# Kernel optimization log

Measured on AMD Instinct MI355X. Metric: run time of the kernel, lower is better.

Reference implementation:

```python
import jax, jax.numpy as jnp
import numpy as np

MX, SX = 0.0, 1.0  # msx
MY, SY = 0.0, 1.0  # msy


def _mode_linear(inp, phase, w, b):
    # Equivalent to: w_p = einsum('ji,imk->jmk', phase, w); out = squeeze(inp[:,None,:] @ w_p) + phase @ b
    # Fused blended form avoids the (batch, in, out) per-sample weight intermediate.
    out = jnp.einsum('bd,idh,bi->bh', inp, w, phase)
    return out + phase @ b


def setup_inputs() -> dict:
    key = jax.random.key(0)
    ks = jax.random.split(key, 4)
    B, D_IN, H, D_OUT = 32768, 256, 1024, 64
    x = jax.random.normal(ks[0], (B, D_IN + 2), dtype=jnp.float32)
    w1 = jax.random.normal(ks[1], (2, D_IN, H), dtype=jnp.float32) * 0.05
    b1 = jnp.zeros((2, H), dtype=jnp.float32)
    w2 = jax.random.normal(ks[2], (2, H, H), dtype=jnp.float32) * 0.05
    b2 = jnp.zeros((2, H), dtype=jnp.float32)
    w3 = jax.random.normal(ks[3], (2, H, D_OUT), dtype=jnp.float32) * 0.05
    b3 = jnp.zeros((2, D_OUT), dtype=jnp.float32)
    return {"x": x, "w1": w1, "b1": b1, "w2": w2, "b2": b2, "w3": w3, "b3": b3}


def reference(x, w1, b1, w2, b2, w3, b3):
    phase = x[:, -2:]                 # unscaled phase weights, per original code
    xs = (x - MX) / SX
    h = xs[:, :-2]                    # [B, D_IN]
    out = jax.nn.elu(_mode_linear(h, phase, w1, b1))
    out = jax.nn.elu(_mode_linear(out, phase, w2, b2))
    out = _mode_linear(out, phase, w3, b3)
    return out * SY + MY
```

## Files before the change

kernel.cpp:

```cpp
#include <hip/hip_runtime.h>

typedef unsigned short u16;
typedef __bf16 bf16x8 __attribute__((ext_vector_type(8)));
typedef float f32x4 __attribute__((ext_vector_type(4)));

static __device__ __forceinline__ u16 f2bf(float f) {
  union { float f; unsigned u; } v; v.f = f;
  unsigned r = (v.u + 0x7fff + ((v.u >> 16) & 1)) >> 16;
  return (u16)r;
}

__global__ void prep_x_kernel(const float* __restrict__ x, u16* __restrict__ hx,
                              float2* __restrict__ phase, int B) {
  int i = blockIdx.x * blockDim.x + threadIdx.x;
  int total = B * 128;
  if (i < total) {
    int row = i >> 7, k2 = (i & 127);
    const float2 v = *reinterpret_cast<const float2*>(x + (size_t)row * 258 + k2 * 2);
    u16 a = f2bf(v.x), b = f2bf(v.y);
    *reinterpret_cast<unsigned*>(hx + (size_t)row * 256 + k2 * 2) =
        (unsigned)a | ((unsigned)b << 16);
  }
  if (i < B) {
    phase[i] = *reinterpret_cast<const float2*>(x + (size_t)i * 258 + 256);
  }
}

__global__ void prep_w_kernel(const float* __restrict__ w, u16* __restrict__ wt,
                              int K, int N) {
  __shared__ u16 tile[64][65];
  int k0 = blockIdx.x * 64, n0 = blockIdx.y * 64, mode = blockIdx.z;
  const float* src = w + (size_t)mode * K * N;
  u16* dst = wt + (size_t)mode * N * K;
  int c = threadIdx.x & 63;
  int r4 = threadIdx.x >> 6;
#pragma unroll
  for (int i = 0; i < 16; ++i) {
    int r = r4 + i * 4;
    tile[r][c] = f2bf(src[(size_t)(k0 + r) * N + n0 + c]);
  }
  __syncthreads();
#pragma unroll
  for (int i = 0; i < 16; ++i) {
    int r = r4 + i * 4;
    dst[(size_t)(n0 + r) * K + k0 + c] = tile[c][r];
  }
}

template <int BM, int BN, int WM, int WN, bool ELU_BF16>
__launch_bounds__(256, 2) __global__
void gemm_dualmode(const u16* __restrict__ A, const u16* __restrict__ WT,
                   const float* __restrict__ bias, const float2* __restrict__ phase,
                   void* __restrict__ out, int K, int N) {
  constexpr int MF = WM / 16, NF = WN / 16;
  __shared__ u16 ldsA[BM * 32];
  __shared__ u16 ldsB[2][BN * 32];
  const int m0 = blockIdx.x * BM;
  const int n0 = blockIdx.y * BN;
  const int t = threadIdx.x;
  const int wave = t >> 6, lane = t & 63;
  constexpr int NWC = BN / WN;
  const int wr = wave / NWC, wc = wave % NWC;
  const int lr = lane & 15, ks = lane >> 4;

  f32x4 acc[2][MF][NF] = {};

  for (int kt = 0; kt < K; kt += 32) {
#pragma unroll
    for (int i = 0; i < BM / 64; ++i) {
      int tt = t + i * 256;
      int r = tt >> 2, c8 = (tt & 3) * 8;
      __builtin_amdgcn_global_load_lds(
          (const __attribute__((address_space(1))) void*)(A + (size_t)(m0 + r) * K + kt + c8),
          (__attribute__((address_space(3))) void*)(ldsA + (size_t)tt * 8), 16, 0, 0);
    }
#pragma unroll
    for (int md = 0; md < 2; ++md) {
#pragma unroll
      for (int i = 0; i < BN / 64; ++i) {
        int tt = t + i * 256;
        int r = tt >> 2, c8 = (tt & 3) * 8;
        __builtin_amdgcn_global_load_lds(
            (const __attribute__((address_space(1))) void*)(WT + (size_t)md * N * K +
                                                            (size_t)(n0 + r) * K + kt + c8),
            (__attribute__((address_space(3))) void*)(ldsB[md] + (size_t)tt * 8), 16, 0, 0);
      }
    }
    __syncthreads();

    bf16x8 af[MF], b0f[NF], b1f[NF];
#pragma unroll
    for (int m = 0; m < MF; ++m)
      af[m] = *reinterpret_cast<const bf16x8*>(&ldsA[(wr * WM + m * 16 + lr) * 32 + ks * 8]);
#pragma unroll
    for (int n = 0; n < NF; ++n) {
      b0f[n] = *reinterpret_cast<const bf16x8*>(&ldsB[0][(wc * WN + n * 16 + lr) * 32 + ks * 8]);
      b1f[n] = *reinterpret_cast<const bf16x8*>(&ldsB[1][(wc * WN + n * 16 + lr) * 32 + ks * 8]);
    }
#pragma unroll
    for (int m = 0; m < MF; ++m) {
#pragma unroll
      for (int n = 0; n < NF; ++n) {
        acc[0][m][n] = __builtin_amdgcn_mfma_f32_16x16x32_bf16(af[m], b0f[n], acc[0][m][n], 0, 0, 0);
        acc[1][m][n] = __builtin_amdgcn_mfma_f32_16x16x32_bf16(af[m], b1f[n], acc[1][m][n], 0, 0, 0);
      }
    }
    __syncthreads();
  }

#pragma unroll
  for (int m = 0; m < MF; ++m) {
#pragma unroll
    for (int j = 0; j < 4; ++j) {
      int grow = m0 + wr * WM + m * 16 + ks * 4 + j;
      float2 ph = phase[grow];
#pragma unroll
      for (int n = 0; n < NF; ++n) {
        int gcol = n0 + wc * WN + n * 16 + lr;
        float v = ph.x * (acc[0][m][n][j] + bias[gcol]) +
                  ph.y * (acc[1][m][n][j] + bias[N + gcol]);
        if (ELU_BF16) {
          v = v > 0.f ? v : (__expf(v) - 1.f);
          ((u16*)out)[(size_t)grow * N + gcol] = f2bf(v);
        } else {
          ((float*)out)[(size_t)grow * N + gcol] = v;
        }
      }
    }
  }
}

extern "C" void kernel_launch(void* const* d_in, const int* in_sizes, int n_in,
                              void* d_out, int out_size, void* d_ws, size_t ws_size,
                              hipStream_t stream) {
  const float* x  = (const float*)d_in[0];
  const float* w1 = (const float*)d_in[1];
  const float* b1 = (const float*)d_in[2];
  const float* w2 = (const float*)d_in[3];
  const float* b2 = (const float*)d_in[4];
  const float* w3 = (const float*)d_in[5];
  const float* b3 = (const float*)d_in[6];
  float* out = (float*)d_out;
  const int B = 32768, DIN = 256, H = 1024, DOUT = 64;

  char* ws = (char*)d_ws;
  u16* W1T = (u16*)ws;     ws += (size_t)2 * H * DIN * 2;
  u16* W2T = (u16*)ws;     ws += (size_t)2 * H * H * 2;
  u16* W3T = (u16*)ws;     ws += (size_t)2 * DOUT * H * 2;
  float2* phase = (float2*)ws; ws += (size_t)B * 8;
  u16* hx = (u16*)ws;      ws += (size_t)B * DIN * 2;
  u16* h1 = (u16*)ws;      ws += (size_t)B * H * 2;
  u16* h2 = (u16*)ws;      ws += (size_t)B * H * 2;

  prep_x_kernel<<<(B * 128 + 255) / 256, 256, 0, stream>>>(x, hx, phase, B);
  prep_w_kernel<<<dim3(DIN / 64, H / 64, 2), 256, 0, stream>>>(w1, W1T, DIN, H);
  prep_w_kernel<<<dim3(H / 64, H / 64, 2), 256, 0, stream>>>(w2, W2T, H, H);
  prep_w_kernel<<<dim3(H / 64, DOUT / 64, 2), 256, 0, stream>>>(w3, W3T, H, DOUT);

  gemm_dualmode<128, 128, 64, 64, true>
      <<<dim3(B / 128, H / 128), 256, 0, stream>>>(hx, W1T, b1, phase, h1, DIN, H);
  gemm_dualmode<128, 128, 64, 64, true>
      <<<dim3(B / 128, H / 128), 256, 0, stream>>>(h1, W2T, b2, phase, h2, H, H);
  gemm_dualmode<128, 64, 64, 32, false>
      <<<dim3(B / 128, DOUT / 64), 256, 0, stream>>>(h2, W3T, b3, phase, out, H, DOUT);
}
```

Measured before the change: 263.1 us.

## Add interleaved-mode 256x256 GEMM with double-buffered LDS and swizzle for layers 1-2

```diff
diff --git a/kernel.cpp b/kernel.cpp
--- a/kernel.cpp
+++ b/kernel.cpp
@@ -3,6 +3,9 @@
 typedef unsigned short u16;
 typedef __bf16 bf16x8 __attribute__((ext_vector_type(8)));
 typedef float f32x4 __attribute__((ext_vector_type(4)));
+
+#define AS1 __attribute__((address_space(1)))
+#define AS3 __attribute__((address_space(3)))
 
 static __device__ __forceinline__ u16 f2bf(float f) {
   union { float f; unsigned u; } v; v.f = f;
@@ -45,6 +48,166 @@
     int r = r4 + i * 4;
     dst[(size_t)(n0 + r) * K + k0 + c] = tile[c][r];
   }
+}
+
+__global__ void prep_w_int_kernel(const float* __restrict__ w, u16* __restrict__ wt,
+                                  int K, int N) {
+  __shared__ u16 tile[64][65];
+  int k0 = blockIdx.x * 64, n0 = blockIdx.y * 64, mode = blockIdx.z;
+  const float* src = w + (size_t)mode * K * N;
+  int c = threadIdx.x & 63;
+  int r4 = threadIdx.x >> 6;
+#pragma unroll
+  for (int i = 0; i < 16; ++i) {
+    int r = r4 + i * 4;
+    tile[r][c] = f2bf(src[(size_t)(k0 + r) * N + n0 + c]);
+  }
+  __syncthreads();
+#pragma unroll
+  for (int i = 0; i < 16; ++i) {
+    int n = n0 + r4 + i * 4;
+    int np = ((n >> 4) << 5) + (mode << 4) + (n & 15);
+    wt[(size_t)np * K + k0 + c] = tile[c][r4 + i * 4];
+  }
+}
+
+template <bool ELU_STORE>
+__global__ __launch_bounds__(512, 2) void gemm8p(
+    const u16* __restrict__ A, const u16* __restrict__ Wt,
+    const float* __restrict__ bias, const float2* __restrict__ phase,
+    u16* __restrict__ out, int K, int Np) {
+  __shared__ u16 lds[2][2][16384];
+  const int tnc = Np >> 8;
+  const int nwg = gridDim.x;
+  int id = blockIdx.x;
+  const int cpx = nwg >> 3;
+  id = (id & 7) * cpx + (id >> 3);
+  const int m0 = (id / tnc) * 256;
+  const int n0 = (id % tnc) * 256;
+  const int t = threadIdx.x;
+  const int lane = t & 63;
+  const int wave = t >> 6;
+  const int wr = wave >> 2, wc = wave & 3;
+  const int lr = lane & 15, ks = lane >> 4;
+  const int cswz = lr * 64 + ((((ks * 8) ^ (((lane >> 3) & 1) << 4))) << 1);
+
+  int soff[4];
+#pragma unroll
+  for (int ld = 0; ld < 4; ++ld) {
+    int e = (ld * 512 + t) * 8;
+    int cp8 = e & 31;
+    int rl = (e >> 5) & 15;
+    int st = e >> 9;
+    int r = ((st >> 1) << 4) + rl;
+    int c0 = ((st & 1) << 5) + (cp8 ^ (((rl >> 3) & 1) << 4));
+    soff[ld] = r * K + c0;
+  }
+  const u16* Abase = A + (size_t)m0 * K;
+  const u16* Bbase = Wt + (size_t)n0 * K;
+
+  f32x4 acc[8][4] = {};
+  const int NT = K >> 6;
+
+  auto stage = [&](int bb, int kt) {
+#pragma unroll
+    for (int ld = 0; ld < 4; ++ld)
+      __builtin_amdgcn_global_load_lds(
+          (const AS1 void*)(Abase + kt + soff[ld]),
+          (AS3 void*)(&lds[bb][0][(ld * 512 + t) * 8]), 16, 0, 0);
+#pragma unroll
+    for (int ld = 0; ld < 4; ++ld)
+      __builtin_amdgcn_global_load_lds(
+          (const AS1 void*)(Bbase + kt + soff[ld]),
+          (AS3 void*)(&lds[bb][1][(ld * 512 + t) * 8]), 16, 0, 0);
+  };
+
+#define BAR()                         \
+  asm volatile("" ::: "memory");      \
+  __builtin_amdgcn_s_barrier();       \
+  asm volatile("" ::: "memory");
+
+  stage(0, 0);
+  asm volatile("s_waitcnt vmcnt(0)" ::: "memory");
+  BAR();
+
+  for (int tt = 0; tt < NT; ++tt) {
+    const int b = tt & 1;
+    const char* lA = (const char*)&lds[b][0][0];
+    const char* lB = (const char*)&lds[b][1][0];
+    bf16x8 af[4][2], bfr[2][2];
+
+#define LOADA(mh)                                                             \
+  _Pragma("unroll") for (int m = 0; m < 4; ++m)                               \
+  _Pragma("unroll") for (int kk = 0; kk < 2; ++kk)                            \
+      af[m][kk] = *(const bf16x8*)(lA +                                       \
+          ((((wr * 8 + (mh)*4 + m) * 2 + kk) << 10) + cswz));
+#define LOADB(nh)                                                             \
+  _Pragma("unroll") for (int n = 0; n < 2; ++n)                               \
+  _Pragma("unroll") for (int kk = 0; kk < 2; ++kk)                            \
+      bfr[n][kk] = *(const bf16x8*)(lB +                                      \
+          ((((wc * 4 + (nh)*2 + n) * 2 + kk) << 10) + cswz));
+#define MFMAQ(mh, nh)                                                         \
+  __builtin_amdgcn_s_setprio(1);                                              \
+  _Pragma("unroll") for (int m = 0; m < 4; ++m)                               \
+  _Pragma("unroll") for (int n = 0; n < 2; ++n)                               \
+  _Pragma("unroll") for (int kk = 0; kk < 2; ++kk)                            \
+      acc[(mh)*4 + m][(nh)*2 + n] = __builtin_amdgcn_mfma_f32_16x16x32_bf16(  \
+          af[m][kk], bfr[n][kk], acc[(mh)*4 + m][(nh)*2 + n], 0, 0, 0);       \
+  __builtin_amdgcn_s_setprio(0);
+
+    LOADA(0); LOADB(0);
+    if (tt + 1 < NT) stage(b ^ 1, (tt + 1) << 6);
+    BAR();
+    __builtin_amdgcn_sched_barrier(0);
+    MFMAQ(0, 0);
+    BAR();
+    LOADB(1);
+    BAR();
+    __builtin_amdgcn_sched_barrier(0);
+    MFMAQ(0, 1);
+    BAR();
+    LOADA(1);
+    BAR();
+    __builtin_amdgcn_sched_barrier(0);
+    MFMAQ(1, 1);
+    BAR();
+    LOADB(0);
+    BAR();
+    __builtin_amdgcn_sched_barrier(0);
+    MFMAQ(1, 0);
+    asm volatile("s_waitcnt vmcnt(0)" ::: "memory");
+    BAR();
+#undef LOADA
+#undef LOADB
+#undef MFMAQ
+  }
+
+  const int Nreal = Np >> 1;
+  const int colbase = (n0 + wc * 64) >> 1;
+  float bias0[2], bias1[2];
+#pragma unroll
+  for (int pj = 0; pj < 2; ++pj) {
+    int ncol = colbase + pj * 16 + lr;
+    bias0[pj] = bias[ncol];
+    bias1[pj] = bias[Nreal + ncol];
+  }
+#pragma unroll
+  for (int m = 0; m < 8; ++m) {
+#pragma unroll
+    for (int j = 0; j < 4; ++j) {
+      int grow = m0 + wr * 128 + m * 16 + ks * 4 + j;
+      float2 ph = phase[grow];
+#pragma unroll
+      for (int pj = 0; pj < 2; ++pj) {
+        int ncol = colbase + pj * 16 + lr;
+        float v = ph.x * (acc[m][pj * 2 + 0][j] + bias0[pj]) +
+                  ph.y * (acc[m][pj * 2 + 1][j] + bias1[pj]);
+        if (ELU_STORE) v = v > 0.f ? v : (__expf(v) - 1.f);
+        out[(size_t)grow * Nreal + ncol] = f2bf(v);
+      }
+    }
+  }
+#undef BAR
 }
 
 template <int BM, int BN, int WM, int WN, bool ELU_BF16>
@@ -71,8 +234,8 @@
       int tt = t + i * 256;
       int r = tt >> 2, c8 = (tt & 3) * 8;
       __builtin_amdgcn_global_load_lds(
-          (const __attribute__((address_space(1))) void*)(A + (size_t)(m0 + r) * K + kt + c8),
-          (__attribute__((address_space(3))) void*)(ldsA + (size_t)tt * 8), 16, 0, 0);
+          (const AS1 void*)(A + (size_t)(m0 + r) * K + kt + c8),
+          (AS3 void*)(ldsA + (size_t)tt * 8), 16, 0, 0);
     }
 #pragma unroll
     for (int md = 0; md < 2; ++md) {
@@ -81,9 +244,8 @@
         int tt = t + i * 256;
         int r = tt >> 2, c8 = (tt & 3) * 8;
         __builtin_amdgcn_global_load_lds(
-            (const __attribute__((address_space(1))) void*)(WT + (size_t)md * N * K +
-                                                            (size_t)(n0 + r) * K + kt + c8),
-            (__attribute__((address_space(3))) void*)(ldsB[md] + (size_t)tt * 8), 16, 0, 0);
+            (const AS1 void*)(WT + (size_t)md * N * K + (size_t)(n0 + r) * K + kt + c8),
+            (AS3 void*)(ldsB[md] + (size_t)tt * 8), 16, 0, 0);
       }
     }
     __syncthreads();
@@ -144,8 +306,8 @@
   const int B = 32768, DIN = 256, H = 1024, DOUT = 64;
 
   char* ws = (char*)d_ws;
-  u16* W1T = (u16*)ws;     ws += (size_t)2 * H * DIN * 2;
-  u16* W2T = (u16*)ws;     ws += (size_t)2 * H * H * 2;
+  u16* W1Ti = (u16*)ws;    ws += (size_t)2 * H * DIN * 2;
+  u16* W2Ti = (u16*)ws;    ws += (size_t)2 * H * H * 2;
   u16* W3T = (u16*)ws;     ws += (size_t)2 * DOUT * H * 2;
   float2* phase = (float2*)ws; ws += (size_t)B * 8;
   u16* hx = (u16*)ws;      ws += (size_t)B * DIN * 2;
@@ -153,14 +315,13 @@
   u16* h2 = (u16*)ws;      ws += (size_t)B * H * 2;
 
   prep_x_kernel<<<(B * 128 + 255) / 256, 256, 0, stream>>>(x, hx, phase, B);
-  prep_w_kernel<<<dim3(DIN / 64, H / 64, 2), 256, 0, stream>>>(w1, W1T, DIN, H);
-  prep_w_kernel<<<dim3(H / 64, H / 64, 2), 256, 0, stream>>>(w2, W2T, H, H);
+  prep_w_int_kernel<<<dim3(DIN / 64, H / 64, 2), 256, 0, stream>>>(w1, W1Ti, DIN, H);
+  prep_w_int_kernel<<<dim3(H / 64, H / 64, 2), 256, 0, stream>>>(w2, W2Ti, H, H);
   prep_w_kernel<<<dim3(H / 64, DOUT / 64, 2), 256, 0, stream>>>(w3, W3T, H, DOUT);
 
-  gemm_dualmode<128, 128, 64, 64, true>
-      <<<dim3(B / 128, H / 128), 256, 0, stream>>>(hx, W1T, b1, phase, h1, DIN, H);
-  gemm_dualmode<128, 128, 64, 64, true>
-      <<<dim3(B / 128, H / 128), 256, 0, stream>>>(h1, W2T, b2, phase, h2, H, H);
+  const int nwg = (B / 256) * (2 * H / 256);
+  gemm8p<true><<<nwg, 512, 0, stream>>>(hx, W1Ti, b1, phase, h1, DIN, 2 * H);
+  gemm8p<true><<<nwg, 512, 0, stream>>>(h1, W2Ti, b2, phase, h2, H, 2 * H);
   gemm_dualmode<128, 64, 64, 32, false>
       <<<dim3(B / 128, DOUT / 64), 256, 0, stream>>>(h2, W3T, b3, phase, out, H, DOUT);
 }
```

Result: faster. 240.6 us (-8.5%).
